# Kernel optimization log

Measured on AMD Instinct MI355X. Metric: run time of the kernel, lower is better.

Reference implementation:

```python
import jax, jax.numpy as jnp
import numpy as np
from jax import lax

T, N, E = 12, 20000, 320000          # timesteps, nodes/graph, edges/graph
F_IN, H_GCN, H_LSTM, N_CLS = 128, 256, 256, 8
NUM_GRAPHS = 1                        # one graph per snapshot (batch all zeros)


def setup_inputs() -> dict:
    key = jax.random.key(0)
    ks = jax.random.split(key, 12)
    s = 0.05
    return {
        "x": jax.random.normal(ks[0], (T, N, F_IN), jnp.float32),
        "edge_index": jax.random.randint(ks[1], (T, 2, E), 0, N, dtype=jnp.int32),
        "batch": jnp.zeros((T, N), jnp.int32),
        "W1": jax.random.normal(ks[2], (F_IN, H_GCN), jnp.float32) * s,
        "b1": jnp.zeros((H_GCN,), jnp.float32),
        "W2": jax.random.normal(ks[3], (H_GCN, H_GCN), jnp.float32) * s,
        "b2": jnp.zeros((H_GCN,), jnp.float32),
        "Wih0": jax.random.normal(ks[4], (4 * H_LSTM, H_GCN), jnp.float32) * s,
        "Whh0": jax.random.normal(ks[5], (4 * H_LSTM, H_LSTM), jnp.float32) * s,
        "bih0": jnp.zeros((4 * H_LSTM,), jnp.float32),
        "bhh0": jnp.zeros((4 * H_LSTM,), jnp.float32),
        "Wih1": jax.random.normal(ks[6], (4 * H_LSTM, H_LSTM), jnp.float32) * s,
        "Whh1": jax.random.normal(ks[7], (4 * H_LSTM, H_LSTM), jnp.float32) * s,
        "bih1": jnp.zeros((4 * H_LSTM,), jnp.float32),
        "bhh1": jnp.zeros((4 * H_LSTM,), jnp.float32),
        "Wlin": jax.random.normal(ks[8], (N_CLS, H_LSTM), jnp.float32) * s,
        "blin": jnp.zeros((N_CLS,), jnp.float32),
    }


def gcn_conv(x, src, dst, W, b, n):
    """PyG GCNConv: linear -> add self-loops -> sym-norm gather/scale/scatter-add + bias."""
    loop = jnp.arange(n, dtype=src.dtype)
    src = jnp.concatenate([src, loop])
    dst = jnp.concatenate([dst, loop])
    deg = jax.ops.segment_sum(jnp.ones(dst.shape, x.dtype), dst, num_segments=n)
    dinv = jnp.where(deg > 0, lax.rsqrt(deg), 0.0)
    norm = dinv[src] * dinv[dst]                       # [E+N]
    xl = x @ W                                         # [N, H]
    out = jax.ops.segment_sum(xl[src] * norm[:, None], dst, num_segments=n)
    return out + b


def lstm_layer(xs, Wih, Whh, bih, bhh):
    """Single-direction LSTM over xs [T, D]; PyTorch gate order i,f,g,o."""
    H = Whh.shape[1]
    bias = bih + bhh

    def step(carry, x):
        h, c = carry
        gates = x @ Wih.T + h @ Whh.T + bias
        i, f, g, o = jnp.split(gates, 4, axis=-1)
        c = jax.nn.sigmoid(f) * c + jax.nn.sigmoid(i) * jnp.tanh(g)
        h = jax.nn.sigmoid(o) * jnp.tanh(c)
        return (h, c), h

    h0 = jnp.zeros((H,), xs.dtype)
    (_, _), hs = lax.scan(step, (h0, h0), xs)
    return hs


def reference(x, edge_index, batch, W1, b1, W2, b2,
              Wih0, Whh0, bih0, bhh0, Wih1, Whh1, bih1, bhh1, Wlin, blin):
    def gcn_step(_, inp):
        xt, et, bt = inp
        h = jax.nn.relu(gcn_conv(xt, et[0], et[1], W1, b1, N))
        h = jax.nn.relu(gcn_conv(h, et[0], et[1], W2, b2, N))
        sums = jax.ops.segment_sum(h, bt, num_segments=NUM_GRAPHS)
        cnt = jax.ops.segment_sum(jnp.ones((N,), h.dtype), bt, num_segments=NUM_GRAPHS)
        return 0, sums / cnt[:, None]                  # global_mean_pool -> [NUM_GRAPHS, H_GCN]

    _, pooled = lax.scan(gcn_step, 0, (x, edge_index, batch))
    seq = pooled.reshape(T * NUM_GRAPHS, H_GCN)        # cat(dim=0) of per-step embeddings
    h1 = lstm_layer(seq, Wih0, Whh0, bih0, bhh0)
    h2 = lstm_layer(h1, Wih1, Whh1, bih1, bhh1)
    return (h2[-1] @ Wlin.T + blin)[None, :]           # [1, N_CLS]
```

## Files before the change

kernel.cpp:

```cpp
#include <hip/hip_runtime.h>
#include <hip/hip_bf16.h>
#include <math.h>

#define T_STEPS 12
#define NNODES  20000
#define NEDGES  320000
#define MPAD    20032
#define FIN     128
#define HG      256
#define RS_STRIDE 20032
#define CHK     16
#define HALF    10000

typedef unsigned short u16;
typedef unsigned int   u32;
typedef unsigned char  u8;
typedef unsigned long long u64;
using bf16x8 = __attribute__((ext_vector_type(8))) short;
using f32x4  = __attribute__((ext_vector_type(4))) float;
typedef float v2f __attribute__((ext_vector_type(2)));

__device__ __forceinline__ float bf2f(u16 u) {
    union { u32 i; float f; } v; v.i = ((u32)u) << 16; return v.f;
}
__device__ __forceinline__ u16 f2bf(float f) {
    union { float f; u32 i; } v; v.f = f;
    u32 r = v.i + 0x7fffu + ((v.i >> 16) & 1u);
    return (u16)(r >> 16);
}
__device__ __forceinline__ u16 f2h(float f) {
    _Float16 h = (_Float16)f; u16 u; __builtin_memcpy(&u, &h, 2); return u;
}
__device__ __forceinline__ float h2f(u16 u) {
    _Float16 h; __builtin_memcpy(&h, &u, 2); return (float)h;
}
__device__ __forceinline__ void gload16(const void* g, void* l) {
    __builtin_amdgcn_global_load_lds(
        (const __attribute__((address_space(1))) u32*)g,
        (__attribute__((address_space(3))) u32*)l, 16, 0, 0);
}
__device__ __forceinline__ float sigm(float x) { return 1.f / (1.f + expf(-x)); }


__global__ void __launch_bounds__(1024) hist2(const int* __restrict__ edges,
        u8* __restrict__ rank, u8* __restrict__ counts) {
    __shared__ u32 lh[HALF];
    int c = blockIdx.x & 15;
    int rest = blockIdx.x >> 4;
    int s = rest & 1, t = rest >> 1;
    for (int i = threadIdx.x; i < HALF; i += 1024) lh[i] = 0;
    __syncthreads();
    int lo = s * HALF;
    const int* db = edges + (size_t)t * 2 * NEDGES + NEDGES;
    u8* rk = rank + (size_t)t * NEDGES;
    int per = NEDGES / CHK;
    int e0 = c * per, e1 = e0 + per;
    for (int i = e0 + (int)threadIdx.x; i < e1; i += 1024) {
        int d = db[i] - lo;
        if ((unsigned)d < HALF) {
            u32 r = atomicAdd(&lh[d], 1u);
            rk[i] = (u8)r;
        }
    }
    __syncthreads();
    u8* cnt = counts + (((size_t)(t * 2 + s) * CHK + c) * HALF);
    for (int i = threadIdx.x; i < HALF; i += 1024) cnt[i] = (u8)lh[i];
}

__global__ void __launch_bounds__(1024) scan2(const u8* __restrict__ counts,
        int* __restrict__ rowstart, float* __restrict__ dinv,
        int* __restrict__ chunkoff) {
    int t = blockIdx.x;
    int tid = threadIdx.x;
    int wid = tid >> 6, lane = tid & 63;
    __shared__ int wsum[16];
    __shared__ int carry_s;
    if (tid == 0) carry_s = 0;
    __syncthreads();
    for (int base = 0; base < NNODES; base += 1024) {
        int i = base + tid;
        int cl[CHK];
        int orig = 0;
        if (i < NNODES) {
            int s = i / HALF, np = i - s * HALF;
            const u8* cp = counts + ((size_t)(t * 2 + s) * CHK) * HALF + np;
#pragma unroll
            for (int c = 0; c < CHK; ++c) { cl[c] = cp[c * HALF]; orig += cl[c]; }
        }
        int v = orig;
#pragma unroll
        for (int off = 1; off < 64; off <<= 1) {
            int n = __shfl_up(v, off);
            if (lane >= off) v += n;
        }
        if (lane == 63) wsum[wid] = v;
        __syncthreads();
        if (wid == 0 && lane < 16) {
            int s = wsum[lane];
#pragma unroll
            for (int off = 1; off < 16; off <<= 1) {
                int n = __shfl_up(s, off);
                if (lane >= off) s += n;
            }
            wsum[lane] = s;
        }
        __syncthreads();
        int incl = v + (wid > 0 ? wsum[wid - 1] : 0) + carry_s;
        int excl = incl - orig;
        if (i < NNODES) {
            rowstart[t * RS_STRIDE + i] = excl;
            dinv[t * NNODES + i] = rsqrtf((float)(orig + 1));
            int s = i / HALF, np = i - s * HALF;
            int* op = chunkoff + ((size_t)(t * 2 + s) * CHK) * HALF + np;
            int run = excl;
#pragma unroll
            for (int c = 0; c < CHK; ++c) { op[c * HALF] = run; run += cl[c]; }
        }
        __syncthreads();
        if (tid == 0) carry_s += wsum[15];
        __syncthreads();
    }
    if (tid == 0) rowstart[t * RS_STRIDE + NNODES] = carry_s;
}

__global__ void __launch_bounds__(1024) fill2(const int* __restrict__ edges,
        const u8* __restrict__ rank, const int* __restrict__ chunkoff,
        int* __restrict__ col) {
    __shared__ int loff[HALF];
    int c = blockIdx.x & 15;
    int rest = blockIdx.x >> 4;
    int s = rest & 1, t = rest >> 1;
    const int* op = chunkoff + (((size_t)(t * 2 + s) * CHK + c) * HALF);
    for (int i = threadIdx.x; i < HALF; i += 1024) loff[i] = op[i];
    __syncthreads();
    int lo = s * HALF;
    const int* sb = edges + (size_t)t * 2 * NEDGES;
    const int* db = sb + NEDGES;
    const u8* rk = rank + (size_t)t * NEDGES;
    int* ct = col + (size_t)t * NEDGES;
    int per = NEDGES / CHK;
    int e0 = c * per, e1 = e0 + per;
    for (int i = e0 + (int)threadIdx.x; i < e1; i += 1024) {
        int d = db[i] - lo;
        if ((unsigned)d < HALF)
            ct[loff[d] + (int)rk[i]] = sb[i];
    }
}


__global__ void __launch_bounds__(256) convall(
        const float* __restrict__ x, const float* __restrict__ dinv, u8* __restrict__ xb,
        const float* __restrict__ W1, u16* __restrict__ W1t,
        const float* __restrict__ W2, u16* __restrict__ W2t,
        float* __restrict__ pooled, u64* __restrict__ hbuf) {
    int bid = blockIdx.x;
    int tid = threadIdx.x;
    if (bid < 30000) {
        int idx = bid * 256 + tid;
        int row = idx >> 5, q = idx & 31;
        float dn = dinv[row];
        float4 v = *(const float4*)&x[(size_t)row * FIN + q * 4];
        int p = __builtin_amdgcn_cvt_pk_fp8_f32(dn * v.x, dn * v.y, 0, false);
        p = __builtin_amdgcn_cvt_pk_fp8_f32(dn * v.z, dn * v.w, p, true);
        ((u32*)xb)[(size_t)row * 32 + q] = (u32)p;
    } else if (bid < 30128) {
        int idx = (bid - 30000) * 256 + tid;
        int n = idx / FIN, k = idx - n * FIN;
        W1t[idx] = f2bf(W1[k * HG + n]);
    } else if (bid < 30384) {
        int idx = (bid - 30128) * 256 + tid;
        int n = idx >> 8, k = idx & 255;
        W2t[idx] = f2bf(W2[k * HG + n]);
    } else {
        for (int i = tid; i < T_STEPS * HG; i += 256) pooled[i] = 0.f;
        for (int i = tid; i < 512; i += 256) hbuf[i] = 0ull;
    }
}


__global__ void __launch_bounds__(256) agg128(const u8* __restrict__ xb,
        const int* __restrict__ rowstart, const int* __restrict__ col,
        const float* __restrict__ dinv, u16* __restrict__ out) {
    int glob = (blockIdx.x << 2) + (threadIdx.x >> 6);
    int lane = threadIdx.x & 63;
    int t = glob / MPAD, node = glob - t * MPAD;
    u16* orow = out + ((size_t)glob) * FIN;
    if (node >= NNODES) { *(u32*)&orow[lane << 1] = 0; return; }
    const u8* xt = xb + (size_t)t * NNODES * FIN;
    const int* cb = col + (size_t)t * NEDGES;
    int o2 = lane << 1;
    u32 pv = *(const u16*)&xt[(size_t)node * FIN + o2];
    v2f f = __builtin_amdgcn_cvt_pk_f32_fp8((int)pv, false);
    float ax = f[0], ay = f[1];
    int s0 = rowstart[t * RS_STRIDE + node], s1 = rowstart[t * RS_STRIDE + node + 1];
    int e = s0;
    for (; e + 16 <= s1; e += 16) {
        int ix[16]; u32 rv[16];
#pragma unroll
        for (int j = 0; j < 16; ++j) ix[j] = cb[e + j];
#pragma unroll
        for (int j = 0; j < 16; ++j) rv[j] = *(const u16*)&xt[(size_t)ix[j] * FIN + o2];
#pragma unroll
        for (int j = 0; j < 16; ++j) {
            v2f g = __builtin_amdgcn_cvt_pk_f32_fp8((int)rv[j], false);
            ax += g[0]; ay += g[1];
        }
    }
    for (; e + 4 <= s1; e += 4) {
        int ix[4]; u32 rv[4];
#pragma unroll
        for (int j = 0; j < 4; ++j) ix[j] = cb[e + j];
#pragma unroll
        for (int j = 0; j < 4; ++j) rv[j] = *(const u16*)&xt[(size_t)ix[j] * FIN + o2];
#pragma unroll
        for (int j = 0; j < 4; ++j) {
            v2f g = __builtin_amdgcn_cvt_pk_f32_fp8((int)rv[j], false);
            ax += g[0]; ay += g[1];
        }
    }
    for (; e < s1; ++e) {
        u32 rv = *(const u16*)&xt[(size_t)cb[e] * FIN + o2];
        v2f g = __builtin_amdgcn_cvt_pk_f32_fp8((int)rv, false);
        ax += g[0]; ay += g[1];
    }
    float dn = dinv[t * NNODES + node];
    u32 packed = (u32)f2bf(dn * ax) | ((u32)f2bf(dn * ay) << 16);
    *(u32*)&orow[o2] = packed;
}

__global__ void __launch_bounds__(256) agg256(const u8* __restrict__ xin,
        const int* __restrict__ rowstart, const int* __restrict__ col,
        const float* __restrict__ dinv, u16* __restrict__ out) {
    int glob = (blockIdx.x << 2) + (threadIdx.x >> 6);
    int lane = threadIdx.x & 63;
    int t = glob / MPAD, node = glob - t * MPAD;
    u16* orow = out + ((size_t)glob) * HG;
    if (node >= NNODES) { *(ushort4*)&orow[lane << 2] = make_ushort4(0, 0, 0, 0); return; }
    const u8* xt = xin + (size_t)t * MPAD * HG;
    const int* cb = col + (size_t)t * NEDGES;
    int o4 = lane << 2;
    u32 pv = *(const u32*)&xt[(size_t)node * HG + o4];
    v2f f01 = __builtin_amdgcn_cvt_pk_f32_fp8((int)pv, false);
    v2f f23 = __builtin_amdgcn_cvt_pk_f32_fp8((int)pv, true);
    float a0 = f01[0], a1 = f01[1], a2 = f23[0], a3 = f23[1];
    int s0 = rowstart[t * RS_STRIDE + node], s1 = rowstart[t * RS_STRIDE + node + 1];
    int e = s0;
    for (; e + 16 <= s1; e += 16) {
        int ix[16]; u32 rv[16];
#pragma unroll
        for (int j = 0; j < 16; ++j) ix[j] = cb[e + j];
#pragma unroll
        for (int j = 0; j < 16; ++j) rv[j] = *(const u32*)&xt[(size_t)ix[j] * HG + o4];
#pragma unroll
        for (int j = 0; j < 16; ++j) {
            v2f g01 = __builtin_amdgcn_cvt_pk_f32_fp8((int)rv[j], false);
            v2f g23 = __builtin_amdgcn_cvt_pk_f32_fp8((int)rv[j], true);
            a0 += g01[0]; a1 += g01[1]; a2 += g23[0]; a3 += g23[1];
        }
    }
    for (; e + 4 <= s1; e += 4) {
        int ix[4]; u32 rv[4];
#pragma unroll
        for (int j = 0; j < 4; ++j) ix[j] = cb[e + j];
#pragma unroll
        for (int j = 0; j < 4; ++j) rv[j] = *(const u32*)&xt[(size_t)ix[j] * HG + o4];
#pragma unroll
        for (int j = 0; j < 4; ++j) {
            v2f g01 = __builtin_amdgcn_cvt_pk_f32_fp8((int)rv[j], false);
            v2f g23 = __builtin_amdgcn_cvt_pk_f32_fp8((int)rv[j], true);
            a0 += g01[0]; a1 += g01[1]; a2 += g23[0]; a3 += g23[1];
        }
    }
    for (; e < s1; ++e) {
        u32 rv = *(const u32*)&xt[(size_t)cb[e] * HG + o4];
        v2f g01 = __builtin_amdgcn_cvt_pk_f32_fp8((int)rv, false);
        v2f g23 = __builtin_amdgcn_cvt_pk_f32_fp8((int)rv, true);
        a0 += g01[0]; a1 += g01[1]; a2 += g23[0]; a3 += g23[1];
    }
    float dn = dinv[t * NNODES + node];
    ushort4 o;
    o.x = f2bf(dn * a0); o.y = f2bf(dn * a1); o.z = f2bf(dn * a2); o.w = f2bf(dn * a3);
    *(ushort4*)&orow[o4] = o;
}


template <int K, bool POOL>
__global__ __launch_bounds__(256) void gemm_bf16(
        const u16* __restrict__ A, const u16* __restrict__ Bt,
        const float* __restrict__ bias, const float* __restrict__ dscale,
        u8* __restrict__ C, float* __restrict__ pool) {
    __shared__ u16 As[64 * 64];
    __shared__ u16 Bs[256 * 64];
    __shared__ float csum[HG];
    int tid = threadIdx.x;
    int bm = blockIdx.x * 64;
    int t8 = tid >> 3, sl = tid & 7;
    int lane = tid & 63, w = tid >> 6;
    int r0 = lane & 15, gq = lane >> 4;
    int tblk = blockIdx.x / 313;

    f32x4 acc[4][4] = {};

    for (int k0 = 0; k0 < K; k0 += 64) {
#pragma unroll
        for (int i = 0; i < 2; ++i) {
            int r = i * 32 + t8;
            int ch = sl ^ (r & 7);
            gload16(A + (size_t)(bm + r) * K + k0 + ch * 8, &As[i * 2048 + tid * 8]);
        }
#pragma unroll
        for (int i = 0; i < 8; ++i) {
            int r = i * 32 + t8;
            int ch = sl ^ (r & 7);
            gload16(Bt + (size_t)r * K + k0 + ch * 8, &Bs[i * 2048 + tid * 8]);
        }
        __syncthreads();
#pragma unroll
        for (int kk = 0; kk < 2; ++kk) {
            bf16x8 a[4], b[4];
#pragma unroll
            for (int mi = 0; mi < 4; ++mi) {
                int R = mi * 16 + r0;
                int s = (kk * 4 + gq) ^ (R & 7);
                a[mi] = *(const bf16x8*)&As[R * 64 + s * 8];
            }
#pragma unroll
            for (int ni = 0; ni < 4; ++ni) {
                int R = w * 64 + ni * 16 + r0;
                int s = (kk * 4 + gq) ^ (R & 7);
                b[ni] = *(const bf16x8*)&Bs[R * 64 + s * 8];
            }
#pragma unroll
            for (int mi = 0; mi < 4; ++mi)
#pragma unroll
                for (int ni = 0; ni < 4; ++ni)
                    acc[mi][ni] = __builtin_amdgcn_mfma_f32_16x16x32_bf16(
                        a[mi], b[ni], acc[mi][ni], 0, 0, 0);
        }
        __syncthreads();
    }

    if (!POOL) {
#pragma unroll
        for (int ni = 0; ni < 4; ++ni) {
            int colg = w * 64 + ni * 16 + r0;
            float b = bias[colg];
#pragma unroll
            for (int mi = 0; mi < 4; ++mi) {
                int rbase = bm + mi * 16 + gq * 4;
#pragma unroll
                for (int q = 0; q < 4; ++q) {
                    int row = rbase + q;
                    int rloc = row - tblk * MPAD;
                    float sc = (rloc < NNODES) ? dscale[tblk * NNODES + rloc] : 0.f;
                    float val = sc * fmaxf(acc[mi][ni][q] + b, 0.f);
                    int p = __builtin_amdgcn_cvt_pk_fp8_f32(val, val, 0, false);
                    C[(size_t)row * HG + colg] = (u8)(p & 0xff);
                }
            }
        }
    } else {
        csum[tid] = 0.f;
        __syncthreads();
#pragma unroll
        for (int ni = 0; ni < 4; ++ni) {
            int colg = w * 64 + ni * 16 + r0;
            float b = bias[colg];
            float s = 0.f;
#pragma unroll
            for (int mi = 0; mi < 4; ++mi) {
                int rbase = bm + mi * 16 + gq * 4;
#pragma unroll
                for (int q = 0; q < 4; ++q) {
                    int row = rbase + q;
                    int rloc = row - tblk * MPAD;
                    if (rloc < NNODES) s += fmaxf(acc[mi][ni][q] + b, 0.f);
                }
            }
            atomicAdd(&csum[colg], s);
        }
        __syncthreads();
        atomicAdd(&pool[tblk * HG + tid], csum[tid]);
    }
}


__global__ void __launch_bounds__(256, 1) lstm4c(
        const float* __restrict__ pooled,
        const float* __restrict__ Wih0, const float* __restrict__ bih0,
        const float* __restrict__ bhh0,
        const float* __restrict__ Whh0, const float* __restrict__ Wih1,
        const float* __restrict__ Whh1,
        const float* __restrict__ bih1, const float* __restrict__ bhh1,
        const float* __restrict__ Wlin, const float* __restrict__ blin,
        u64* hbuf, float* __restrict__ out) {
    if (blockIdx.x & 7) return;
    __shared__ float xs[T_STEPS][HG];
    __shared__ float hseqL[T_STEPS][HG];
    __shared__ float hl[HG];
    __shared__ float garr[256];
    int tid = threadIdx.x;
    int b = blockIdx.x >> 3;
    int lu = tid & 63;
    int unit = b * 64 + lu;
    int r = (tid >> 6) * 256 + unit;

    for (int i = tid; i < T_STEPS * HG; i += 256)
        ((float*)xs)[i] = pooled[i] * (1.f / (float)NNODES);
    __syncthreads();

    float pre[T_STEPS];
    {
        const float4* w4 = (const float4*)(Wih0 + (size_t)r * HG);
#pragma unroll
        for (int t = 0; t < T_STEPS; ++t) pre[t] = 0.f;
        for (int i = 0; i < 64; ++i) {
            float4 wv = w4[i];
#pragma unroll
            for (int t = 0; t < T_STEPS; ++t) {
                float4 xv = *(const float4*)&xs[t][i * 4];
                pre[t] += wv.x * xv.x + wv.y * xv.y + wv.z * xv.z + wv.w * xv.w;
            }
        }
        float bb = bih0[r] + bhh0[r];
#pragma unroll
        for (int t = 0; t < T_STEPS; ++t) pre[t] += bb;
    }

    u32 wreg[128];
    for (int layer = 0; layer < 2; ++layer) {
        const float* Whh = layer ? Whh1 : Whh0;
        {
            const float4* w4 = (const float4*)(Whh + (size_t)r * HG);
#pragma unroll
            for (int i = 0; i < 64; ++i) {
                float4 v = w4[i];
                wreg[2 * i]     = (u32)f2h(v.x) | ((u32)f2h(v.y) << 16);
                wreg[2 * i + 1] = (u32)f2h(v.z) | ((u32)f2h(v.w) << 16);
            }
        }
        float c = 0.f;
        hl[tid] = 0.f;
        __syncthreads();
        for (int t = 0; t < T_STEPS; ++t) {
            int s = layer * T_STEPS + t + 1;
            float acc = 0.f;
#pragma unroll
            for (int k2 = 0; k2 < 128; ++k2) {
                u32 wv = wreg[k2];
                float2 hv = *(const float2*)&hl[k2 * 2];
                acc += h2f((u16)wv) * hv.x + h2f((u16)(wv >> 16)) * hv.y;
            }
            garr[tid] = pre[t] + acc;
            __syncthreads();
            if (tid < 64) {
                float ig = sigm(garr[lu]);
                float fg = sigm(garr[64 + lu]);
                float gg = tanhf(garr[128 + lu]);
                float og = sigm(garr[192 + lu]);
                c = fg * c + ig * gg;
                float hn = og * tanhf(c);
                u32 hb; __builtin_memcpy(&hb, &hn, 4);
                u64 pk = ((u64)(u32)s << 32) | (u64)hb;
                __hip_atomic_store(&hbuf[(s & 1) * 256 + unit], pk,
                                   __ATOMIC_RELAXED, __HIP_MEMORY_SCOPE_AGENT);
            }
            u64 v;
            do {
                v = __hip_atomic_load(&hbuf[(s & 1) * 256 + tid],
                                      __ATOMIC_RELAXED, __HIP_MEMORY_SCOPE_AGENT);
            } while ((u32)(v >> 32) != (u32)s);
            u32 lo = (u32)v;
            float hv; __builtin_memcpy(&hv, &lo, 4);
            __syncthreads();
            hl[tid] = hv;
            if (layer == 0) hseqL[t][tid] = hv;
            __syncthreads();
        }
        if (layer == 0) {
            const float4* w4 = (const float4*)(Wih1 + (size_t)r * HG);
#pragma unroll
            for (int t = 0; t < T_STEPS; ++t) pre[t] = 0.f;
            for (int i = 0; i < 64; ++i) {
                float4 wv = w4[i];
#pragma unroll
                for (int t = 0; t < T_STEPS; ++t) {
                    float4 hv = *(const float4*)&hseqL[t][i * 4];
                    pre[t] += wv.x * hv.x + wv.y * hv.y + wv.z * hv.z + wv.w * hv.w;
                }
            }
            float bb = bih1[r] + bhh1[r];
#pragma unroll
            for (int t = 0; t < T_STEPS; ++t) pre[t] += bb;
            __syncthreads();
        }
    }

    if (b == 0 && tid < 8) {
        float s = blin[tid];
        const float* wl = Wlin + tid * HG;
        for (int k = 0; k < HG; ++k) s += hl[k] * wl[k];
        out[tid] = s;
    }
}


extern "C" void kernel_launch(void* const* d_in, const int* in_sizes, int n_in,
                              void* d_out, int out_size, void* d_ws, size_t ws_size,
                              hipStream_t stream) {
    const float* x    = (const float*)d_in[0];
    const int*   edges= (const int*)d_in[1];
    const float* W1   = (const float*)d_in[3];
    const float* b1   = (const float*)d_in[4];
    const float* W2   = (const float*)d_in[5];
    const float* b2   = (const float*)d_in[6];
    const float* Wih0 = (const float*)d_in[7];
    const float* Whh0 = (const float*)d_in[8];
    const float* bih0 = (const float*)d_in[9];
    const float* bhh0 = (const float*)d_in[10];
    const float* Wih1 = (const float*)d_in[11];
    const float* Whh1 = (const float*)d_in[12];
    const float* bih1 = (const float*)d_in[13];
    const float* bhh1 = (const float*)d_in[14];
    const float* Wlin = (const float*)d_in[15];
    const float* blin = (const float*)d_in[16];
    (void)in_sizes; (void)n_in; (void)out_size;

    char* p = (char*)d_ws;
    auto alloc = [&](size_t bytes) -> char* {
        char* q = p; p += (bytes + 255) & ~(size_t)255; return q;
    };
    int*   rowstart = (int*)  alloc(sizeof(int)   * T_STEPS * RS_STRIDE);
    float* dinv     = (float*)alloc(sizeof(float) * T_STEPS * NNODES);
    int*   col      = (int*)  alloc(sizeof(int)   * T_STEPS * NEDGES);
    u8*    rank     = (u8*)   alloc((size_t)T_STEPS * NEDGES);
    u8*    counts   = (u8*)   alloc((size_t)T_STEPS * 2 * CHK * HALF);
    int*   chunkoff = (int*)  alloc(sizeof(int)   * (size_t)T_STEPS * 2 * CHK * HALF);
    float* pooled   = (float*)alloc(sizeof(float) * T_STEPS * HG);
    u16*   W1t      = (u16*)  alloc(sizeof(u16)   * HG * FIN);
    u16*   W2t      = (u16*)  alloc(sizeof(u16)   * HG * HG);
    u64*   hbuf     = (u64*)  alloc(sizeof(u64)   * 2 * 256);
    size_t fixed_used = (size_t)(p - (char*)d_ws);

    const size_t xb_bytes  = (size_t)T_STEPS * NNODES * FIN;
    const size_t per_g     = (size_t)MPAD * HG * (1 + 2);
    const size_t slack     = 4096 * 16;
    static const int gopts[6] = {12, 6, 4, 3, 2, 1};
    int G = 1;
    for (int i = 0; i < 6; ++i)
        if (fixed_used + xb_bytes + per_g * gopts[i] + slack <= ws_size) { G = gopts[i]; break; }
    u8*  xb   = (u8*) alloc(xb_bytes);
    u8*  h1b  = (u8*) alloc((size_t)G * MPAD * HG);
    u16* aggu = (u16*)alloc(sizeof(u16) * (size_t)G * MPAD * HG);

    hist2<<<T_STEPS * 2 * CHK, 1024, 0, stream>>>(edges, rank, counts);
    scan2<<<T_STEPS, 1024, 0, stream>>>(counts, rowstart, dinv, chunkoff);
    fill2<<<T_STEPS * 2 * CHK, 1024, 0, stream>>>(edges, rank, chunkoff, col);
    convall<<<30385, 256, 0, stream>>>(x, dinv, xb, W1, W1t, W2, W2t, pooled, hbuf);

    for (int g = 0; g < T_STEPS / G; ++g) {
        int t0 = g * G;
        const u8*    xbg = xb + (size_t)t0 * NNODES * FIN;
        const int*   rsg = rowstart + (size_t)t0 * RS_STRIDE;
        const int*   clg = col + (size_t)t0 * NEDGES;
        const float* dvg = dinv + (size_t)t0 * NNODES;
        int nagg = G * MPAD / 4;
        agg128<<<nagg, 256, 0, stream>>>(xbg, rsg, clg, dvg, aggu);
        gemm_bf16<FIN, false><<<G * 313, 256, 0, stream>>>(aggu, W1t, b1, dvg,
                h1b, nullptr);
        agg256<<<nagg, 256, 0, stream>>>(h1b, rsg, clg, dvg, aggu);
        gemm_bf16<HG, true><<<G * 313, 256, 0, stream>>>(aggu, W2t, b2, nullptr,
                nullptr, pooled + (size_t)t0 * HG);
    }
    lstm4c<<<25, 256, 0, stream>>>(pooled, Wih0, bih0, bhh0, Whh0, Wih1, Whh1,
                                   bih1, bhh1, Wlin, blin, hbuf, (float*)d_out);
}
```

Before: 765.0 us.

## Pre-pack LSTM weights to fp16 transposed layout and exchange hidden state as bf16

The LSTM weight conversion to packed fp16 moves into the existing conversion kernel, stored transposed so each thread's loads are coalesced across rows. The LSTM kernel now launches exactly 4 blocks instead of 25 with 21 idle, and reads the pre-packed weights. Cross-block hidden-state exchange packs two bf16 values per 64-bit slot, with each block reading only the other blocks' slots and polling with a sleep. This trades some hidden-state precision (bf16 rounding) for less traffic and latency in the serial recurrence.

```diff
diff --git a/kernel.cpp b/kernel.cpp
--- a/kernel.cpp
+++ b/kernel.cpp
@@ -152,6 +152,9 @@
         const float* __restrict__ x, const float* __restrict__ dinv, u8* __restrict__ xb,
         const float* __restrict__ W1, u16* __restrict__ W1t,
         const float* __restrict__ W2, u16* __restrict__ W2t,
+        const float* __restrict__ Wih0, const float* __restrict__ Whh0,
+        const float* __restrict__ Wih1, const float* __restrict__ Whh1,
+        u32* __restrict__ lw,
         float* __restrict__ pooled, u64* __restrict__ hbuf) {
     int bid = blockIdx.x;
     int tid = threadIdx.x;
@@ -171,9 +174,18 @@
         int idx = (bid - 30128) * 256 + tid;
         int n = idx >> 8, k = idx & 255;
         W2t[idx] = f2bf(W2[k * HG + n]);
+    } else if (bid == 30384) {
+        for (int i = tid; i < T_STEPS * HG; i += 256) pooled[i] = 0.f;
+        for (int i = tid; i < 256; i += 256) hbuf[i] = 0ull;
     } else {
-        for (int i = tid; i < T_STEPS * HG; i += 256) pooled[i] = 0.f;
-        for (int i = tid; i < 512; i += 256) hbuf[i] = 0ull;
+        int idx = bid - 30385;
+        int m = idx >> 10, r = idx & 1023;
+        const float* src = (m == 0) ? Wih0 : (m == 1) ? Whh0 : (m == 2) ? Wih1 : Whh1;
+        if (tid < 128) {
+            float2 w2 = *(const float2*)&src[(size_t)r * HG + tid * 2];
+            lw[((size_t)m * 128 + tid) * 1024 + r] =
+                (u32)f2h(w2.x) | ((u32)f2h(w2.y) << 16);
+        }
     }
 }
 
@@ -385,22 +397,18 @@
 }
 
 
-__global__ void __launch_bounds__(256, 1) lstm4c(
-        const float* __restrict__ pooled,
-        const float* __restrict__ Wih0, const float* __restrict__ bih0,
-        const float* __restrict__ bhh0,
-        const float* __restrict__ Whh0, const float* __restrict__ Wih1,
-        const float* __restrict__ Whh1,
+__global__ void __launch_bounds__(256, 1) lstm4d(
+        const float* __restrict__ pooled, const u32* __restrict__ lw,
+        const float* __restrict__ bih0, const float* __restrict__ bhh0,
         const float* __restrict__ bih1, const float* __restrict__ bhh1,
         const float* __restrict__ Wlin, const float* __restrict__ blin,
         u64* hbuf, float* __restrict__ out) {
-    if (blockIdx.x & 7) return;
     __shared__ float xs[T_STEPS][HG];
     __shared__ float hseqL[T_STEPS][HG];
     __shared__ float hl[HG];
     __shared__ float garr[256];
     int tid = threadIdx.x;
-    int b = blockIdx.x >> 3;
+    int b = blockIdx.x;
     int lu = tid & 63;
     int unit = b * 64 + lu;
     int r = (tid >> 6) * 256 + unit;
@@ -411,16 +419,15 @@
 
     float pre[T_STEPS];
     {
-        const float4* w4 = (const float4*)(Wih0 + (size_t)r * HG);
+        const u32* wp = lw + r;
 #pragma unroll
         for (int t = 0; t < T_STEPS; ++t) pre[t] = 0.f;
-        for (int i = 0; i < 64; ++i) {
-            float4 wv = w4[i];
-#pragma unroll
-            for (int t = 0; t < T_STEPS; ++t) {
-                float4 xv = *(const float4*)&xs[t][i * 4];
-                pre[t] += wv.x * xv.x + wv.y * xv.y + wv.z * xv.z + wv.w * xv.w;
-            }
+        for (int k = 0; k < 128; ++k) {
+            u32 pk = wp[(size_t)k * 1024];
+            float w0 = h2f((u16)pk), w1 = h2f((u16)(pk >> 16));
+#pragma unroll
+            for (int t = 0; t < T_STEPS; ++t)
+                pre[t] += w0 * xs[t][2 * k] + w1 * xs[t][2 * k + 1];
         }
         float bb = bih0[r] + bhh0[r];
 #pragma unroll
@@ -429,15 +436,10 @@
 
     u32 wreg[128];
     for (int layer = 0; layer < 2; ++layer) {
-        const float* Whh = layer ? Whh1 : Whh0;
         {
-            const float4* w4 = (const float4*)(Whh + (size_t)r * HG);
-#pragma unroll
-            for (int i = 0; i < 64; ++i) {
-                float4 v = w4[i];
-                wreg[2 * i]     = (u32)f2h(v.x) | ((u32)f2h(v.y) << 16);
-                wreg[2 * i + 1] = (u32)f2h(v.z) | ((u32)f2h(v.w) << 16);
-            }
+            const u32* wp = lw + (size_t)((layer ? 3 : 1) * 128) * 1024 + r;
+#pragma unroll
+            for (int k = 0; k < 128; ++k) wreg[k] = wp[(size_t)k * 1024];
         }
         float c = 0.f;
         hl[tid] = 0.f;
@@ -446,9 +448,9 @@
             int s = layer * T_STEPS + t + 1;
             float acc = 0.f;
 #pragma unroll
-            for (int k2 = 0; k2 < 128; ++k2) {
-                u32 wv = wreg[k2];
-                float2 hv = *(const float2*)&hl[k2 * 2];
+            for (int k = 0; k < 128; ++k) {
+                u32 wv = wreg[k];
+                float2 hv = *(const float2*)&hl[k * 2];
                 acc += h2f((u16)wv) * hv.x + h2f((u16)(wv >> 16)) * hv.y;
             }
             garr[tid] = pre[t] + acc;
@@ -460,34 +462,42 @@
                 float og = sigm(garr[192 + lu]);
                 c = fg * c + ig * gg;
                 float hn = og * tanhf(c);
-                u32 hb; __builtin_memcpy(&hb, &hn, 4);
-                u64 pk = ((u64)(u32)s << 32) | (u64)hb;
-                __hip_atomic_store(&hbuf[(s & 1) * 256 + unit], pk,
-                                   __ATOMIC_RELAXED, __HIP_MEMORY_SCOPE_AGENT);
-            }
-            u64 v;
-            do {
-                v = __hip_atomic_load(&hbuf[(s & 1) * 256 + tid],
-                                      __ATOMIC_RELAXED, __HIP_MEMORY_SCOPE_AGENT);
-            } while ((u32)(v >> 32) != (u32)s);
-            u32 lo = (u32)v;
-            float hv; __builtin_memcpy(&hv, &lo, 4);
+                u16 hb16 = f2bf(hn);
+                hl[unit] = bf2f(hb16);
+                if (lu < 32) {
+                    u16 h0 = f2bf(hl[b * 64 + 2 * lu]);
+                    u16 h1 = f2bf(hl[b * 64 + 2 * lu + 1]);
+                    u64 pk = ((u64)(u32)s << 32) | (u32)h0 | ((u32)h1 << 16);
+                    __hip_atomic_store(&hbuf[(s & 1) * 128 + b * 32 + lu], pk,
+                                       __ATOMIC_RELAXED, __HIP_MEMORY_SCOPE_AGENT);
+                }
+            }
+            if (tid < 128 && (tid >> 5) != b) {
+                u64 v = __hip_atomic_load(&hbuf[(s & 1) * 128 + tid],
+                                          __ATOMIC_RELAXED, __HIP_MEMORY_SCOPE_AGENT);
+                while ((u32)(v >> 32) != (u32)s) {
+                    __builtin_amdgcn_s_sleep(1);
+                    v = __hip_atomic_load(&hbuf[(s & 1) * 128 + tid],
+                                          __ATOMIC_RELAXED, __HIP_MEMORY_SCOPE_AGENT);
+                }
+                u32 lo = (u32)v;
+                hl[2 * tid]     = bf2f((u16)lo);
+                hl[2 * tid + 1] = bf2f((u16)(lo >> 16));
+            }
             __syncthreads();
-            hl[tid] = hv;
-            if (layer == 0) hseqL[t][tid] = hv;
+            if (layer == 0) hseqL[t][tid] = hl[tid];
+        }
+        if (layer == 0) {
             __syncthreads();
-        }
-        if (layer == 0) {
-            const float4* w4 = (const float4*)(Wih1 + (size_t)r * HG);
+            const u32* wp = lw + (size_t)(2 * 128) * 1024 + r;
 #pragma unroll
             for (int t = 0; t < T_STEPS; ++t) pre[t] = 0.f;
-            for (int i = 0; i < 64; ++i) {
-                float4 wv = w4[i];
-#pragma unroll
-                for (int t = 0; t < T_STEPS; ++t) {
-                    float4 hv = *(const float4*)&hseqL[t][i * 4];
-                    pre[t] += wv.x * hv.x + wv.y * hv.y + wv.z * hv.z + wv.w * hv.w;
-                }
+            for (int k = 0; k < 128; ++k) {
+                u32 pk = wp[(size_t)k * 1024];
+                float w0 = h2f((u16)pk), w1 = h2f((u16)(pk >> 16));
+#pragma unroll
+                for (int t = 0; t < T_STEPS; ++t)
+                    pre[t] += w0 * hseqL[t][2 * k] + w1 * hseqL[t][2 * k + 1];
             }
             float bb = bih1[r] + bhh1[r];
 #pragma unroll
@@ -539,7 +549,8 @@
     float* pooled   = (float*)alloc(sizeof(float) * T_STEPS * HG);
     u16*   W1t      = (u16*)  alloc(sizeof(u16)   * HG * FIN);
     u16*   W2t      = (u16*)  alloc(sizeof(u16)   * HG * HG);
-    u64*   hbuf     = (u64*)  alloc(sizeof(u64)   * 2 * 256);
+    u32*   lw       = (u32*)  alloc(sizeof(u32)   * 4 * 128 * 1024);
+    u64*   hbuf     = (u64*)  alloc(sizeof(u64)   * 2 * 128);
     size_t fixed_used = (size_t)(p - (char*)d_ws);
 
     const size_t xb_bytes  = (size_t)T_STEPS * NNODES * FIN;
@@ -556,7 +567,8 @@
     hist2<<<T_STEPS * 2 * CHK, 1024, 0, stream>>>(edges, rank, counts);
     scan2<<<T_STEPS, 1024, 0, stream>>>(counts, rowstart, dinv, chunkoff);
     fill2<<<T_STEPS * 2 * CHK, 1024, 0, stream>>>(edges, rank, chunkoff, col);
-    convall<<<30385, 256, 0, stream>>>(x, dinv, xb, W1, W1t, W2, W2t, pooled, hbuf);
+    convall<<<34481, 256, 0, stream>>>(x, dinv, xb, W1, W1t, W2, W2t,
+                                       Wih0, Whh0, Wih1, Whh1, lw, pooled, hbuf);
 
     for (int g = 0; g < T_STEPS / G; ++g) {
         int t0 = g * G;
@@ -572,6 +584,6 @@
         gemm_bf16<HG, true><<<G * 313, 256, 0, stream>>>(aggu, W2t, b2, nullptr,
                 nullptr, pooled + (size_t)t0 * HG);
     }
-    lstm4c<<<25, 256, 0, stream>>>(pooled, Wih0, bih0, bhh0, Whh0, Wih1, Whh1,
-                                   bih1, bhh1, Wlin, blin, hbuf, (float*)d_out);
-}
+    lstm4d<<<4, 256, 0, stream>>>(pooled, lw, bih0, bhh0, bih1, bhh1, Wlin, blin,
+                                  hbuf, (float*)d_out);
+}
```

Measured after the change: 762.1 us. No clear change (-0.4%).
